# Kernel tuning notes

Measured on AMD Instinct MI355X. Metric: run time of the kernel, lower is better.

## Reference

```python
import jax, jax.numpy as jnp
import numpy as np

EPS = 1e-5


def setup_inputs() -> dict:
    key = jax.random.key(0)
    ks = jax.random.split(key, 6)
    B, H, W, C = 4, 64, 64, 64
    x_in = jax.random.normal(ks[0], (B, H, W, C), dtype=jnp.float32)
    scale = 1.0 / np.sqrt(C)
    w1 = jax.random.normal(ks[1], (C, C), dtype=jnp.float32) * scale
    w2 = jax.random.normal(ks[2], (C, C), dtype=jnp.float32) * scale
    w3 = jax.random.normal(ks[3], (C, C), dtype=jnp.float32) * scale
    w4 = jax.random.normal(ks[4], (C, C), dtype=jnp.float32) * scale
    zeros = jnp.zeros((C,), dtype=jnp.float32)
    return {
        "x_in": x_in,
        "w1": w1, "w2": w2, "w3": w3, "w4": w4,
        "b1": zeros, "b2": zeros, "b3": zeros, "b4": zeros,
        "gamma": jnp.ones((C,), dtype=jnp.float32),
        "beta": zeros,
    }


def reference(x_in, w1, w2, w3, w4, b1, b2, b3, b4, gamma, beta):
    B, H, W, C = x_in.shape
    # BatchNorm over batch + spatial dims, per channel (training-mode batch stats)
    mean = jnp.mean(x_in, axis=(0, 1, 2))            # [C]
    var = jnp.var(x_in, axis=(0, 1, 2))              # [C]
    x = (x_in - mean) * jax.lax.rsqrt(var + EPS) * gamma + beta
    # QKV projections
    q = jnp.einsum('bhwc,cC->bhwC', x, w1) + b1
    k = jnp.einsum('bhwc,cC->bhwC', x, w2) + b2
    v = jnp.einsum('bhwc,cC->bhwC', x, w3) + b3
    # Full spatial attention: [B, H, W, H, W]
    sdpa = jnp.einsum('bhwc,bHWc->bhwHW', q, k) / jnp.sqrt(jnp.float32(C))
    sdpa = jax.nn.softmax(sdpa.reshape(B, H, W, H * W), axis=-1)
    sdpa = sdpa.reshape(B, H, W, H, W)
    x = jnp.einsum('bhwHW,bHWc->bhwc', sdpa, v)
    # Output projection + residual
    x = jnp.einsum('bhwc,cC->bhwC', x, w4) + b4
    return x + x_in
```

## Files before the change

kernel.cpp:

```cpp
#include <hip/hip_runtime.h>

typedef _Float16 f16;
typedef _Float16 half8 __attribute__((ext_vector_type(8)));
typedef float f32x4 __attribute__((ext_vector_type(4)));

#define LDW 72

__global__ __launch_bounds__(256) void k_bnstats(const float* __restrict__ x, float* __restrict__ sums){
    __shared__ float red[512];
    int t = threadIdx.x;
    int c = t & 63, rg = t >> 6;
    int rb = blockIdx.x * 64;
    float s = 0.f, s2 = 0.f;
    for(int r = rg; r < 64; r += 4){
        float v = x[(rb + r) * 64 + c];
        s += v; s2 += v * v;
    }
    red[t] = s; red[256 + t] = s2;
    __syncthreads();
    if(t < 64){
        float a = red[t] + red[t + 64] + red[t + 128] + red[t + 192];
        float b = red[256 + t] + red[256 + t + 64] + red[256 + t + 128] + red[256 + t + 192];
        atomicAdd(&sums[c], a);
        atomicAdd(&sums[64 + c], b);
    }
}

__global__ __launch_bounds__(256) void k_qkv(
    const float* __restrict__ x,
    const float* __restrict__ w1, const float* __restrict__ w2, const float* __restrict__ w3,
    const float* __restrict__ b1, const float* __restrict__ b2, const float* __restrict__ b3,
    const float* __restrict__ gamma, const float* __restrict__ beta,
    const float* __restrict__ sums,
    f16* __restrict__ Q, f16* __restrict__ Kx, f16* __restrict__ Vt){
    __shared__ f16 wT[3 * 64 * LDW];
    __shared__ float sc[64], sh[64], bb[3][64];
    int t = threadIdx.x;
    for(int i = t; i < 3 * 4096; i += 256){
        int j = i >> 12, e = i & 4095, k = e >> 6, n = e & 63;
        const float* wp = (j == 0) ? w1 : ((j == 1) ? w2 : w3);
        wT[j * 64 * LDW + n * LDW + k] = (f16)wp[e];
    }
    if(t < 64){
        float mean = sums[t] * (1.f / 16384.f);
        float var  = sums[64 + t] * (1.f / 16384.f) - mean * mean;
        float s = gamma[t] * rsqrtf(var + 1e-5f);
        sc[t] = s;
        sh[t] = beta[t] - mean * s;
        bb[0][t] = b1[t]; bb[1][t] = b2[t]; bb[2][t] = b3[t];
    }
    __syncthreads();
    int w = t >> 6, lane = t & 63, quad = lane >> 4, l15 = lane & 15;
    int rowb = blockIdx.x * 64 + w * 16;
    int arow = rowb + l15;
    half8 a[2];
    #pragma unroll
    for(int kc = 0; kc < 2; kc++){
        f32x4 x0 = *(const f32x4*)&x[arow * 64 + kc * 32 + quad * 8];
        f32x4 x1 = *(const f32x4*)&x[arow * 64 + kc * 32 + quad * 8 + 4];
        half8 h;
        #pragma unroll
        for(int j = 0; j < 8; j++){
            int c = kc * 32 + quad * 8 + j;
            float xv = (j < 4) ? x0[j & 3] : x1[j & 3];
            h[j] = (f16)(xv * sc[c] + sh[c]);
        }
        a[kc] = h;
    }
    const f32x4 vzero = {0.f, 0.f, 0.f, 0.f};
    f32x4 acc[3][4];
    #pragma unroll
    for(int m = 0; m < 3; m++){
        #pragma unroll
        for(int nt = 0; nt < 4; nt++){
            acc[m][nt] = vzero;
            #pragma unroll
            for(int kc = 0; kc < 2; kc++){
                half8 bfr = *(half8*)&wT[m * 64 * LDW + (nt * 16 + l15) * LDW + kc * 32 + quad * 8];
                acc[m][nt] = __builtin_amdgcn_mfma_f32_16x16x32_f16(a[kc], bfr, acc[m][nt], 0, 0, 0);
            }
        }
    }
    const float qs = 0.18033688011112043f;
    #pragma unroll
    for(int nt = 0; nt < 4; nt++){
        #pragma unroll
        for(int r = 0; r < 4; r++){
            int row = rowb + quad * 4 + r;
            int col = nt * 16 + l15;
            Q[row * 64 + col]  = (f16)((acc[0][nt][r] + bb[0][col]) * qs);
            Kx[row * 64 + col] = (f16)(acc[1][nt][r] + bb[1][col]);
            Vt[((row >> 12) * 64 + col) * 4096 + (row & 4095)] = (f16)(acc[2][nt][r] + bb[2][col]);
        }
    }
}

__global__ __launch_bounds__(256, 2) void k_attn(
    const f16* __restrict__ Q, const f16* __restrict__ Kx, const f16* __restrict__ Vt,
    f16* __restrict__ Oph, float* __restrict__ lw){
    __shared__ f16 Pw[4][16 * LDW];
    int t = threadIdx.x;
    int kq = blockIdx.x & 7, qg = blockIdx.x >> 3;
    int b = qg >> 4;
    int w = t >> 6, lane = t & 63, quad = lane >> 4, l15 = lane & 15;
    int qrow0 = qg * 256 + w * 64;

    half8 aq[4][2];
    #pragma unroll
    for(int rg = 0; rg < 4; rg++)
        #pragma unroll
        for(int kc = 0; kc < 2; kc++)
            aq[rg][kc] = *(const half8*)&Q[(qrow0 + rg * 16 + l15) * 64 + kc * 32 + quad * 8];

    const f32x4 vzero = {0.f, 0.f, 0.f, 0.f};
    f32x4 o[4][4];
    float lp[4][4];
    #pragma unroll
    for(int rg = 0; rg < 4; rg++)
        #pragma unroll
        for(int nt = 0; nt < 4; nt++){ o[rg][nt] = vzero; lp[rg][nt] = 0.f; }

    const f16* kp[4];
    const f16* vp[4];
    #pragma unroll
    for(int nt = 0; nt < 4; nt++){
        kp[nt] = &Kx[(b * 4096 + kq * 8 * 64 + nt * 16 + l15) * 64 + quad * 8];
        vp[nt] = &Vt[(b * 64 + nt * 16 + l15) * 4096 + kq * 8 * 64 + quad * 8];
    }

    for(int j = 0; j < 8; j++){
        half8 kf[4][2], vf[4][2];
        #pragma unroll
        for(int nt = 0; nt < 4; nt++){
            #pragma unroll
            for(int kc = 0; kc < 2; kc++){
                kf[nt][kc] = *(const half8*)(kp[nt] + kc * 32);
                vf[nt][kc] = *(const half8*)(vp[nt] + kc * 32);
            }
            kp[nt] += 64 * 64;
            vp[nt] += 64;
        }
        #pragma unroll
        for(int rg = 0; rg < 4; rg++){
            f32x4 s[4];
            #pragma unroll
            for(int nt = 0; nt < 4; nt++){
                s[nt] = vzero;
                #pragma unroll
                for(int kc = 0; kc < 2; kc++)
                    s[nt] = __builtin_amdgcn_mfma_f32_16x16x32_f16(aq[rg][kc], kf[nt][kc], s[nt], 0, 0, 0);
            }
            #pragma unroll
            for(int nt = 0; nt < 4; nt++){
                #pragma unroll
                for(int r = 0; r < 4; r++){
                    float p = __builtin_amdgcn_exp2f(fminf(s[nt][r], 15.f));
                    lp[rg][r] += p;
                    Pw[w][(quad * 4 + r) * LDW + nt * 16 + l15] = (f16)p;
                }
            }
            #pragma unroll
            for(int kc = 0; kc < 2; kc++){
                half8 pf = *(half8*)&Pw[w][l15 * LDW + kc * 32 + quad * 8];
                #pragma unroll
                for(int nt = 0; nt < 4; nt++)
                    o[rg][nt] = __builtin_amdgcn_mfma_f32_16x16x32_f16(pf, vf[nt][kc], o[rg][nt], 0, 0, 0);
            }
        }
    }
    #pragma unroll
    for(int rg = 0; rg < 4; rg++){
        #pragma unroll
        for(int r = 0; r < 4; r++){
            float v = lp[rg][r];
            v += __shfl_xor(v, 1); v += __shfl_xor(v, 2);
            v += __shfl_xor(v, 4); v += __shfl_xor(v, 8);
            int row = qrow0 + rg * 16 + quad * 4 + r;
            if(l15 == 0) lw[kq * 16384 + row] = v;
            float inv = __builtin_amdgcn_rcpf(v);
            #pragma unroll
            for(int nt = 0; nt < 4; nt++)
                Oph[kq * 1048576 + row * 64 + nt * 16 + l15] = (f16)(o[rg][nt][r] * inv);
        }
    }
}

__global__ __launch_bounds__(256) void k_merge(
    const f16* __restrict__ Oph, const float* __restrict__ lw,
    const float* __restrict__ w4, const float* __restrict__ b4,
    const float* __restrict__ x, float* __restrict__ out){
    __shared__ f16 Om[64 * LDW];
    __shared__ f16 wT[64 * LDW];
    __shared__ float b4f[64];
    int t = threadIdx.x;
    int rb = blockIdx.x * 64;
    for(int i = t; i < 4096; i += 256){
        int k = i >> 6, n = i & 63;
        wT[n * LDW + k] = (f16)w4[i];
    }
    if(t < 64) b4f[t] = b4[t];
    for(int i = t; i < 512; i += 256){
        int row = i >> 3, c8 = i & 7;
        int gr = rb + row;
        float num[8] = {0.f,0.f,0.f,0.f,0.f,0.f,0.f,0.f};
        float den = 0.f;
        #pragma unroll
        for(int s = 0; s < 8; s++){
            float li = lw[s * 16384 + gr];
            half8 ov = *(const half8*)&Oph[s * 1048576 + gr * 64 + c8 * 8];
            #pragma unroll
            for(int j = 0; j < 8; j++) num[j] += li * (float)ov[j];
            den += li;
        }
        float invd = 1.f / den;
        #pragma unroll
        for(int j = 0; j < 8; j++) Om[row * LDW + c8 * 8 + j] = (f16)(num[j] * invd);
    }
    __syncthreads();
    int w = t >> 6, lane = t & 63, quad = lane >> 4, l15 = lane & 15;
    half8 a[2];
    #pragma unroll
    for(int kc = 0; kc < 2; kc++)
        a[kc] = *(half8*)&Om[(w * 16 + l15) * LDW + kc * 32 + quad * 8];
    #pragma unroll
    for(int nt = 0; nt < 4; nt++){
        f32x4 y = {0.f, 0.f, 0.f, 0.f};
        #pragma unroll
        for(int kc = 0; kc < 2; kc++){
            half8 bfr = *(half8*)&wT[(nt * 16 + l15) * LDW + kc * 32 + quad * 8];
            y = __builtin_amdgcn_mfma_f32_16x16x32_f16(a[kc], bfr, y, 0, 0, 0);
        }
        #pragma unroll
        for(int r = 0; r < 4; r++){
            int row = rb + w * 16 + quad * 4 + r;
            int col = nt * 16 + l15;
            out[row * 64 + col] = y[r] + b4f[col] + x[row * 64 + col];
        }
    }
}

extern "C" void kernel_launch(void* const* d_in, const int* in_sizes, int n_in,
                              void* d_out, int out_size, void* d_ws, size_t ws_size,
                              hipStream_t stream){
    (void)in_sizes; (void)n_in; (void)out_size; (void)ws_size;
    const float* x  = (const float*)d_in[0];
    const float* w1 = (const float*)d_in[1];
    const float* w2 = (const float*)d_in[2];
    const float* w3 = (const float*)d_in[3];
    const float* w4 = (const float*)d_in[4];
    const float* b1 = (const float*)d_in[5];
    const float* b2 = (const float*)d_in[6];
    const float* b3 = (const float*)d_in[7];
    const float* b4 = (const float*)d_in[8];
    const float* gm = (const float*)d_in[9];
    const float* bt = (const float*)d_in[10];
    char* ws = (char*)d_ws;
    f16* Q   = (f16*)(ws);
    f16* Kx  = (f16*)(ws + (size_t)(2u << 20));
    f16* Vt  = (f16*)(ws + (size_t)(4u << 20));
    float* sums = (float*)(ws + (size_t)(6u << 20));
    f16* Oph = (f16*)(ws + (size_t)(6u << 20) + 1024);
    float* lwp = (float*)(ws + (size_t)(22u << 20) + 1024);

    hipMemsetAsync(sums, 0, 512, stream);
    hipLaunchKernelGGL(k_bnstats, dim3(256), dim3(256), 0, stream, x, sums);
    hipLaunchKernelGGL(k_qkv,     dim3(256), dim3(256), 0, stream, x, w1, w2, w3, b1, b2, b3, gm, bt, sums, Q, Kx, Vt);
    hipLaunchKernelGGL(k_attn,    dim3(512), dim3(256), 0, stream, Q, Kx, Vt, Oph, lwp);
    hipLaunchKernelGGL(k_merge,   dim3(256), dim3(256), 0, stream, Oph, lwp, w4, b4, x, (float*)d_out);
}
```

Before: 146.4 us.

## Double-buffer K/V register fragments and transpose QK MFMA for packed P stores

The attention kernel now prefetches the next K/V tile into a second register buffer while computing on the current one, and fully unrolls the 8-step loop. It swaps the operands of the QK^T MFMA so each lane holds four consecutive key columns of one query row, which allows a single packed half4 store of P to shared memory instead of four scalar stores. Row-sum reduction now needs only two cross-quad shuffles rather than four. The clamp on the exponent is dropped, and doubling the K/V fragment registers raises register pressure and may lower occupancy.

```diff
diff --git a/kernel.cpp b/kernel.cpp
--- a/kernel.cpp
+++ b/kernel.cpp
@@ -1,6 +1,7 @@
 #include <hip/hip_runtime.h>
 
 typedef _Float16 f16;
+typedef _Float16 half4 __attribute__((ext_vector_type(4)));
 typedef _Float16 half8 __attribute__((ext_vector_type(8)));
 typedef float f32x4 __attribute__((ext_vector_type(4)));
 
@@ -114,70 +115,90 @@
 
     const f32x4 vzero = {0.f, 0.f, 0.f, 0.f};
     f32x4 o[4][4];
-    float lp[4][4];
-    #pragma unroll
-    for(int rg = 0; rg < 4; rg++)
-        #pragma unroll
-        for(int nt = 0; nt < 4; nt++){ o[rg][nt] = vzero; lp[rg][nt] = 0.f; }
+    float lacc[4];
+    #pragma unroll
+    for(int rg = 0; rg < 4; rg++){
+        #pragma unroll
+        for(int nt = 0; nt < 4; nt++) o[rg][nt] = vzero;
+        lacc[rg] = 0.f;
+    }
 
     const f16* kp[4];
     const f16* vp[4];
     #pragma unroll
     for(int nt = 0; nt < 4; nt++){
-        kp[nt] = &Kx[(b * 4096 + kq * 8 * 64 + nt * 16 + l15) * 64 + quad * 8];
-        vp[nt] = &Vt[(b * 64 + nt * 16 + l15) * 4096 + kq * 8 * 64 + quad * 8];
-    }
-
+        kp[nt] = &Kx[(b * 4096 + kq * 512 + nt * 16 + l15) * 64 + quad * 8];
+        vp[nt] = &Vt[(b * 64 + nt * 16 + l15) * 4096 + kq * 512 + quad * 8];
+    }
+
+    half8 kf[2][4][2], vf[2][4][2];
+    #pragma unroll
+    for(int nt = 0; nt < 4; nt++){
+        #pragma unroll
+        for(int kc = 0; kc < 2; kc++){
+            kf[0][nt][kc] = *(const half8*)(kp[nt] + kc * 32);
+            vf[0][nt][kc] = *(const half8*)(vp[nt] + kc * 32);
+        }
+        kp[nt] += 64 * 64;
+        vp[nt] += 64;
+    }
+
+    #pragma unroll
     for(int j = 0; j < 8; j++){
-        half8 kf[4][2], vf[4][2];
-        #pragma unroll
-        for(int nt = 0; nt < 4; nt++){
-            #pragma unroll
-            for(int kc = 0; kc < 2; kc++){
-                kf[nt][kc] = *(const half8*)(kp[nt] + kc * 32);
-                vf[nt][kc] = *(const half8*)(vp[nt] + kc * 32);
-            }
-            kp[nt] += 64 * 64;
-            vp[nt] += 64;
+        int cur = j & 1, nxt = cur ^ 1;
+        if(j < 7){
+            #pragma unroll
+            for(int nt = 0; nt < 4; nt++){
+                #pragma unroll
+                for(int kc = 0; kc < 2; kc++){
+                    kf[nxt][nt][kc] = *(const half8*)(kp[nt] + kc * 32);
+                    vf[nxt][nt][kc] = *(const half8*)(vp[nt] + kc * 32);
+                }
+                kp[nt] += 64 * 64;
+                vp[nt] += 64;
+            }
         }
         #pragma unroll
         for(int rg = 0; rg < 4; rg++){
-            f32x4 s[4];
+            f32x4 st[4];
             #pragma unroll
             for(int nt = 0; nt < 4; nt++){
-                s[nt] = vzero;
+                st[nt] = vzero;
                 #pragma unroll
                 for(int kc = 0; kc < 2; kc++)
-                    s[nt] = __builtin_amdgcn_mfma_f32_16x16x32_f16(aq[rg][kc], kf[nt][kc], s[nt], 0, 0, 0);
+                    st[nt] = __builtin_amdgcn_mfma_f32_16x16x32_f16(kf[cur][nt][kc], aq[rg][kc], st[nt], 0, 0, 0);
             }
             #pragma unroll
             for(int nt = 0; nt < 4; nt++){
-                #pragma unroll
-                for(int r = 0; r < 4; r++){
-                    float p = __builtin_amdgcn_exp2f(fminf(s[nt][r], 15.f));
-                    lp[rg][r] += p;
-                    Pw[w][(quad * 4 + r) * LDW + nt * 16 + l15] = (f16)p;
-                }
-            }
-            #pragma unroll
-            for(int kc = 0; kc < 2; kc++){
-                half8 pf = *(half8*)&Pw[w][l15 * LDW + kc * 32 + quad * 8];
-                #pragma unroll
-                for(int nt = 0; nt < 4; nt++)
-                    o[rg][nt] = __builtin_amdgcn_mfma_f32_16x16x32_f16(pf, vf[nt][kc], o[rg][nt], 0, 0, 0);
-            }
+                float p0 = __builtin_amdgcn_exp2f(st[nt][0]);
+                float p1 = __builtin_amdgcn_exp2f(st[nt][1]);
+                float p2 = __builtin_amdgcn_exp2f(st[nt][2]);
+                float p3 = __builtin_amdgcn_exp2f(st[nt][3]);
+                lacc[rg] += (p0 + p1) + (p2 + p3);
+                half4 pk = { (f16)p0, (f16)p1, (f16)p2, (f16)p3 };
+                *(half4*)&Pw[w][l15 * LDW + nt * 16 + quad * 4] = pk;
+            }
+            half8 pf0 = *(half8*)&Pw[w][l15 * LDW + quad * 8];
+            half8 pf1 = *(half8*)&Pw[w][l15 * LDW + 32 + quad * 8];
+            #pragma unroll
+            for(int nt = 0; nt < 4; nt++)
+                o[rg][nt] = __builtin_amdgcn_mfma_f32_16x16x32_f16(pf0, vf[cur][nt][0], o[rg][nt], 0, 0, 0);
+            #pragma unroll
+            for(int nt = 0; nt < 4; nt++)
+                o[rg][nt] = __builtin_amdgcn_mfma_f32_16x16x32_f16(pf1, vf[cur][nt][1], o[rg][nt], 0, 0, 0);
         }
     }
     #pragma unroll
     for(int rg = 0; rg < 4; rg++){
+        float lt = lacc[rg];
+        lt += __shfl_xor(lt, 16);
+        lt += __shfl_xor(lt, 32);
+        if(quad == 0) lw[kq * 16384 + qrow0 + rg * 16 + l15] = lt;
         #pragma unroll
         for(int r = 0; r < 4; r++){
-            float v = lp[rg][r];
-            v += __shfl_xor(v, 1); v += __shfl_xor(v, 2);
-            v += __shfl_xor(v, 4); v += __shfl_xor(v, 8);
+            float lr = __shfl(lt, quad * 4 + r);
+            float inv = __builtin_amdgcn_rcpf(lr);
             int row = qrow0 + rg * 16 + quad * 4 + r;
-            if(l15 == 0) lw[kq * 16384 + row] = v;
-            float inv = __builtin_amdgcn_rcpf(v);
             #pragma unroll
             for(int nt = 0; nt < 4; nt++)
                 Oph[kq * 1048576 + row * 64 + nt * 16 + l15] = (f16)(o[rg][nt][r] * inv);
@@ -262,7 +283,7 @@
     f16* Oph = (f16*)(ws + (size_t)(6u << 20) + 1024);
     float* lwp = (float*)(ws + (size_t)(22u << 20) + 1024);
 
-    hipMemsetAsync(sums, 0, 512, stream);
+    (void)hipMemsetAsync(sums, 0, 512, stream);
     hipLaunchKernelGGL(k_bnstats, dim3(256), dim3(256), 0, stream, x, sums);
     hipLaunchKernelGGL(k_qkv,     dim3(256), dim3(256), 0, stream, x, w1, w2, w3, b1, b2, b3, gm, bt, sums, Q, Kx, Vt);
     hipLaunchKernelGGL(k_attn,    dim3(512), dim3(256), 0, stream, Q, Kx, Vt, Oph, lwp);
```

Result: slower. 216.5 us (+47.9%).
